# Performance work log

Measured on AMD Instinct MI355X. Metric: run time of the kernel, lower is better.

## Reference

```python
import jax, jax.numpy as jnp
import numpy as np

GROUPS = 1024
K_N = 32
FEAT_DIM = 64
EPS = 1e-05


def farthest_point_sample(xyz, npoint):
    # xyz: [B, N, 3] -> centroids [B, npoint] int32
    # Original torch code starts from a random point; we use index 0 for determinism.
    B, N, _ = xyz.shape

    def step(carry, _):
        distance, farthest = carry
        centroid = jnp.take_along_axis(xyz, farthest[:, None, None], axis=1)  # [B,1,3]
        dist = jnp.sum((xyz - centroid) ** 2, axis=-1)  # [B,N]
        distance = jnp.minimum(distance, dist)
        new_far = jnp.argmax(distance, axis=-1).astype(jnp.int32)
        return (distance, new_far), farthest

    init = (jnp.full((B, N), 1e10, dtype=xyz.dtype), jnp.zeros((B,), jnp.int32))
    _, cents = jax.lax.scan(step, init, None, length=npoint)
    return cents.T  # [B, npoint]


def index_points(points, idx):
    # points: [B, N, C]; idx: [B, ...] -> [B, ..., C]
    B = points.shape[0]
    bidx = jnp.arange(B).reshape((B,) + (1,) * (idx.ndim - 1))
    return points[bidx, idx]


def square_distance(src, dst):
    # src [B,S,C], dst [B,N,C] -> [B,S,N]
    d = -2.0 * jnp.einsum('bsc,bnc->bsn', src, dst)
    d = d + jnp.sum(src ** 2, -1)[:, :, None]
    d = d + jnp.sum(dst ** 2, -1)[:, None, :]
    return d


def setup_inputs() -> dict:
    key = jax.random.key(0)
    k1, k2 = jax.random.split(key)
    xyz = jax.random.normal(k1, (8, 3, 4096), dtype=jnp.float32)
    feats = jax.random.normal(k2, (8, FEAT_DIM, 4096), dtype=jnp.float32)
    affine_alpha_p = jnp.ones((1, 1, 1, FEAT_DIM), jnp.float32)
    affine_beta_p = jnp.zeros((1, 1, 1, FEAT_DIM), jnp.float32)
    return {"xyz": xyz, "feats": feats,
            "affine_alpha_p": affine_alpha_p, "affine_beta_p": affine_beta_p}


def reference(xyz, feats, affine_alpha_p, affine_beta_p):
    xyz = jnp.transpose(xyz, (0, 2, 1))      # [B,N,3]
    feats = jnp.transpose(feats, (0, 2, 1))  # [B,N,D]
    B, N, _ = xyz.shape
    S, k = GROUPS, K_N

    fps_idx = farthest_point_sample(xyz, S)          # [B,S]
    new_xyz = index_points(xyz, fps_idx)             # [B,S,3]
    new_feats = index_points(feats, fps_idx)         # [B,S,D]

    sqr = square_distance(new_xyz, xyz)              # [B,S,N]
    _, idx = jax.lax.top_k(-sqr, k)                  # smallest-k -> [B,S,k]
    grouped = index_points(feats, idx)               # [B,S,k,D]

    mean = new_feats[:, :, None, :]                  # [B,S,1,D]
    diff = grouped - mean
    # torch.std over flattened per-batch, unbiased (ddof=1)
    std = jnp.std(diff.reshape(B, -1), axis=-1, ddof=1)[:, None, None, None]
    grouped = diff / (std + EPS)
    grouped = affine_alpha_p * grouped + affine_beta_p

    point_feats = jnp.concatenate(
        [grouped, grouped - new_feats[:, :, None, :]], axis=-1)  # [B,S,k,2D]

    new_feats_out = jnp.transpose(new_feats, (0, 2, 1))          # [B,D,S]
    new_xyz_out = jnp.transpose(new_xyz, (0, 2, 1))              # [B,3,S]
    point_feats_out = jnp.transpose(point_feats, (0, 3, 1, 2))   # [B,2D,S,k]
    return (new_xyz_out, new_feats_out, point_feats_out)
```

## Files before the change

### kernel.cpp

```cpp
#include <hip/hip_runtime.h>

#define NPTS 4096
#define NSAMP 1024
#define KNN_K 32
#define FDIM 64
#define EPSF 1e-5f

#define DPP_MAX64(CTRL)                                                          \
  {                                                                              \
    unsigned _olo = (unsigned)__builtin_amdgcn_update_dpp(0, (int)klo, CTRL,     \
                                                          0xf, 0xf, true);       \
    unsigned _ohi = (unsigned)__builtin_amdgcn_update_dpp(0, (int)khi, CTRL,     \
                                                          0xf, 0xf, true);       \
    unsigned long long _ok = ((unsigned long long)_ohi << 32) | _olo;            \
    unsigned long long _ck = ((unsigned long long)khi << 32) | klo;              \
    if (_ok > _ck) { klo = _olo; khi = _ohi; }                                   \
  }

__global__ __launch_bounds__(256) void fps_kernel(const float* __restrict__ xyz,
                                                  int* __restrict__ fps_idx,
                                                  float* __restrict__ sqnorm) {
  __shared__ float4 pts[NPTS];
  __shared__ unsigned long long skeys[2][4];
  __shared__ int fpsb[NSAMP];
  const int b = blockIdx.x, t = threadIdx.x;
  const int lane = t & 63, w = t >> 6;
  const float* xb = xyz + (size_t)b * 3 * NPTS;
  float px[16], py[16], pz[16], dist[16];
  unsigned rik[16];
#pragma unroll
  for (int k = 0; k < 16; ++k) {
    int p = k * 256 + t;
    float x = xb[p], y = xb[NPTS + p], z = xb[2 * NPTS + p];
    float sq = __fadd_rn(__fadd_rn(__fmul_rn(x, x), __fmul_rn(y, y)),
                         __fmul_rn(z, z));
    px[k] = x; py[k] = y; pz[k] = z; dist[k] = 1e10f;
    rik[k] = 4095u - (unsigned)p;
    pts[p] = make_float4(x, y, z, sq);
    sqnorm[b * NPTS + p] = sq;
  }
  if (t == 0) fpsb[0] = 0;
  __syncthreads();
  float4 c = pts[0];
  for (int it = 1; it < NSAMP; ++it) {
#pragma unroll
    for (int k = 0; k < 16; ++k) {
      float dx = __fsub_rn(px[k], c.x);
      float dy = __fsub_rn(py[k], c.y);
      float dz = __fsub_rn(pz[k], c.z);
      float dd = __fadd_rn(__fadd_rn(__fmul_rn(dx, dx), __fmul_rn(dy, dy)),
                           __fmul_rn(dz, dz));
      dist[k] = fminf(dist[k], dd);
    }
    float m01 = fmaxf(dist[0], dist[1]),  m23 = fmaxf(dist[2], dist[3]);
    float m45 = fmaxf(dist[4], dist[5]),  m67 = fmaxf(dist[6], dist[7]);
    float m89 = fmaxf(dist[8], dist[9]),  mab = fmaxf(dist[10], dist[11]);
    float mcd = fmaxf(dist[12], dist[13]), mef = fmaxf(dist[14], dist[15]);
    float q0 = fmaxf(m01, m23), q1 = fmaxf(m45, m67);
    float q2 = fmaxf(m89, mab), q3 = fmaxf(mcd, mef);
    float mv = fmaxf(fmaxf(q0, q1), fmaxf(q2, q3));
    unsigned ri = rik[15];
#pragma unroll
    for (int k = 15; k >= 0; --k) ri = (dist[k] == mv) ? rik[k] : ri;
    unsigned bvb = __float_as_uint(mv);
    unsigned klo = (bvb << 12) | ri;
    unsigned khi = bvb >> 20;
    DPP_MAX64(0x111)
    DPP_MAX64(0x112)
    DPP_MAX64(0x114)
    DPP_MAX64(0x118)
    DPP_MAX64(0x142)
    DPP_MAX64(0x143)
    if (lane == 63) skeys[it & 1][w] = ((unsigned long long)khi << 32) | klo;
    __syncthreads();
    unsigned long long kk = skeys[it & 1][lane & 3];
    klo = (unsigned)kk;
    khi = (unsigned)(kk >> 32);
    DPP_MAX64(0x111)
    DPP_MAX64(0x112)
    unsigned flo = (unsigned)__builtin_amdgcn_readlane((int)klo, 3);
    int far = 4095 - (int)(flo & 0xfffu);
    if (t == 0) fpsb[it] = far;
    c = pts[far];
  }
  __syncthreads();
#pragma unroll
  for (int k = 0; k < 4; ++k)
    fps_idx[b * NSAMP + k * 256 + t] = fpsb[k * 256 + t];
}

__global__ __launch_bounds__(256) void gather_feats_kernel(const float* __restrict__ feats,
                                                           const int* __restrict__ fps,
                                                           float* __restrict__ out1,
                                                           float* __restrict__ nf) {
  int i = blockIdx.x * 256 + threadIdx.x;
  int s = i & 1023, c = (i >> 10) & 63, b = i >> 16;
  int p = fps[(b << 10) + s];
  float v = feats[((size_t)(b * 64 + c)) * NPTS + p];
  out1[(b * 64 + c) * 1024 + s] = v;
  nf[(((b << 10) + s) << 6) + c] = v;
}

__global__ __launch_bounds__(256) void gather_xyz_kernel(const float* __restrict__ xyz,
                                                         const float* __restrict__ sqnorm,
                                                         const int* __restrict__ fps,
                                                         float* __restrict__ out0,
                                                         float4* __restrict__ nx4) {
  int i = blockIdx.x * 256 + threadIdx.x;
  int b = i >> 10, s = i & 1023;
  int p = fps[i];
  const float* xb = xyz + (size_t)b * 3 * NPTS;
  float x = xb[p], y = xb[NPTS + p], z = xb[2 * NPTS + p];
  nx4[i] = make_float4(x, y, z, sqnorm[b * NPTS + p]);
  out0[(b * 3 + 0) * 1024 + s] = x;
  out0[(b * 3 + 1) * 1024 + s] = y;
  out0[(b * 3 + 2) * 1024 + s] = z;
}

__device__ __forceinline__ unsigned long long mk_key(float xn, float yn, float zn,
                                                     float sq, float cx, float cy,
                                                     float cz, float src2, int n) {
  float dot = __fmaf_rn(zn, cz, __fmaf_rn(yn, cy, __fmul_rn(xn, cx)));
  float d = __fadd_rn(__fadd_rn(__fmul_rn(-2.0f, dot), src2), sq);
  unsigned mb = __float_as_uint(d);
  mb = (mb & 0x80000000u) ? ~mb : (mb | 0x80000000u);
  return ((unsigned long long)mb << 32) | (unsigned)n;
}

__global__ __launch_bounds__(256, 2) void knn_kernel(const float* __restrict__ xyz,
                                                     const float* __restrict__ sqnorm,
                                                     const float4* __restrict__ nx4,
                                                     int* __restrict__ knn) {
  const int lane = threadIdx.x & 63;
  const int w = threadIdx.x >> 6;
  const int row = blockIdx.x * 4 + w;
  const int b = row >> 10;
  const float4 c4 = nx4[row];
  const float cx = c4.x, cy = c4.y, cz = c4.z, src2 = c4.w;
  const float4* x4 = (const float4*)(xyz + (size_t)b * 3 * NPTS);
  const float4* y4 = (const float4*)(xyz + (size_t)b * 3 * NPTS + NPTS);
  const float4* z4 = (const float4*)(xyz + (size_t)b * 3 * NPTS + 2 * NPTS);
  const float4* s4 = (const float4*)(sqnorm + (size_t)b * NPTS);
  unsigned long long key[64];
#pragma unroll
  for (int jj = 0; jj < 16; ++jj) {
    int vi = jj * 64 + lane;
    float4 xv = x4[vi], yv = y4[vi], zv = z4[vi], sv = s4[vi];
    int n0 = vi * 4;
    key[jj * 4 + 0] = mk_key(xv.x, yv.x, zv.x, sv.x, cx, cy, cz, src2, n0);
    key[jj * 4 + 1] = mk_key(xv.y, yv.y, zv.y, sv.y, cx, cy, cz, src2, n0 + 1);
    key[jj * 4 + 2] = mk_key(xv.z, yv.z, zv.z, sv.z, cx, cy, cz, src2, n0 + 2);
    key[jj * 4 + 3] = mk_key(xv.w, yv.w, zv.w, sv.w, cx, cy, cz, src2, n0 + 3);
  }
  unsigned long long last = 0ull;
  const int out_base = row * KNN_K;
#pragma unroll 1
  for (int r = 0; r < KNN_K; ++r) {
    unsigned long long cur = ~0ull;
#pragma unroll
    for (int j = 0; j < 64; ++j) {
      unsigned long long k = key[j];
      if (k > last && k < cur) cur = k;
    }
#pragma unroll
    for (int off = 32; off > 0; off >>= 1) {
      unsigned long long o = __shfl_xor(cur, off);
      cur = (o < cur) ? o : cur;
    }
    last = cur;
    if (lane == r) knn[out_base + r] = (int)(unsigned)(cur & 0xffffffffull);
  }
}

__global__ __launch_bounds__(256) void stats_kernel(const float* __restrict__ feats,
                                                    const float* __restrict__ nf,
                                                    const int* __restrict__ knn,
                                                    double* __restrict__ stats) {
  const int b = blockIdx.x >> 5;
  const int chunk = blockIdx.x & 31;
  const int base = chunk * 65536;
  double sm = 0.0, sq = 0.0;
  for (int i = 0; i < 256; ++i) {
    int e = base + i * 256 + threadIdx.x;
    int c = e >> 15;
    int sk = e & 32767;
    int s = sk >> 5, j = sk & 31;
    int p = knn[((((b << 10) + s)) << 5) + j];
    float f = feats[((size_t)(b * 64 + c)) * NPTS + p];
    float m = nf[(((b << 10) + s) << 6) + c];
    double d = (double)__fsub_rn(f, m);
    sm += d;
    sq += d * d;
  }
#pragma unroll
  for (int off = 32; off > 0; off >>= 1) {
    sm += __shfl_down(sm, off);
    sq += __shfl_down(sq, off);
  }
  __shared__ double red[8];
  int w = threadIdx.x >> 6;
  if ((threadIdx.x & 63) == 0) { red[w * 2] = sm; red[w * 2 + 1] = sq; }
  __syncthreads();
  if (threadIdx.x == 0) {
    atomicAdd(&stats[b * 2 + 0], red[0] + red[2] + red[4] + red[6]);
    atomicAdd(&stats[b * 2 + 1], red[1] + red[3] + red[5] + red[7]);
  }
}

__global__ __launch_bounds__(256) void out_kernel(const float* __restrict__ feats,
                                                  const float* __restrict__ nf,
                                                  const int* __restrict__ knn,
                                                  const double* __restrict__ stats,
                                                  const float* __restrict__ alpha,
                                                  const float* __restrict__ beta,
                                                  float* __restrict__ out2) {
  const int plane = blockIdx.x;
  const int b = plane >> 6, c = plane & 63;
  const int sk = blockIdx.y * 256 + threadIdx.x;
  const int s = sk >> 5, j = sk & 31;
  const double n = 2097152.0;
  double sm = stats[b * 2], sqs = stats[b * 2 + 1];
  double var = (sqs - sm * sm / n) / (n - 1.0);
  float stdf = (float)sqrt(var);
  float denom = stdf + EPSF;
  int p = knn[((((b << 10) + s)) << 5) + j];
  float f = feats[((size_t)(b * 64 + c)) * NPTS + p];
  float m = nf[(((b << 10) + s) << 6) + c];
  float diff = __fsub_rn(f, m);
  float g = alpha[c] * (diff / denom) + beta[c];
  size_t o1 = (((size_t)(b * 128 + c) << 10) + (size_t)s) * 32 + j;
  size_t o2 = (((size_t)(b * 128 + 64 + c) << 10) + (size_t)s) * 32 + j;
  out2[o1] = g;
  out2[o2] = g - m;
}

extern "C" void kernel_launch(void* const* d_in, const int* in_sizes, int n_in,
                              void* d_out, int out_size, void* d_ws, size_t ws_size,
                              hipStream_t stream) {
  (void)in_sizes; (void)n_in; (void)out_size; (void)ws_size;
  const float* xyz   = (const float*)d_in[0];
  const float* feats = (const float*)d_in[1];
  const float* alpha = (const float*)d_in[2];
  const float* beta  = (const float*)d_in[3];
  float* out  = (float*)d_out;
  float* out0 = out;
  float* out1 = out + 24576;
  float* out2 = out + 24576 + 524288;

  char* ws = (char*)d_ws;
  int*    fps   = (int*)ws;
  float*  sqn   = (float*)(ws + 32768);
  float4* nx4   = (float4*)(ws + 163840);
  float*  nf    = (float*)(ws + 294912);
  int*    knn   = (int*)(ws + 2392064);
  double* stats = (double*)(ws + 3440640);

  hipMemsetAsync(stats, 0, 128, stream);
  fps_kernel<<<8, 256, 0, stream>>>(xyz, fps, sqn);
  gather_feats_kernel<<<2048, 256, 0, stream>>>(feats, fps, out1, nf);
  gather_xyz_kernel<<<32, 256, 0, stream>>>(xyz, sqn, fps, out0, nx4);
  knn_kernel<<<2048, 256, 0, stream>>>(xyz, sqn, nx4, knn);
  stats_kernel<<<256, 256, 0, stream>>>(feats, nf, knn, stats);
  out_kernel<<<dim3(512, 128), 256, 0, stream>>>(feats, nf, knn, stats, alpha, beta, out2);
}
```

Measured before the change: 969.6 us.

## Pack two batches per FPS block and use float-max DPP with ballot argmax

The FPS kernel now runs two batches per 512-thread block (4 blocks instead of 8), and the per-wave argmax reduction is restructured. It first reduces only the float max across the wave with 32-bit DPP ops, then finds the index with a ballot over the 16 register slots. This replaces the 64-bit key DPP reduction and the per-lane index select. It cuts per-iteration ALU work in the serial FPS loop. Sharing one barrier across two batches may add sync coupling, and using fewer CUs gives no extra parallelism.

```diff
diff --git a/kernel.cpp b/kernel.cpp
--- a/kernel.cpp
+++ b/kernel.cpp
@@ -5,6 +5,13 @@
 #define KNN_K 32
 #define FDIM 64
 #define EPSF 1e-5f
+
+#define DPP_FMAX(CTRL)                                                           \
+  {                                                                              \
+    int _o = __builtin_amdgcn_update_dpp(0, __float_as_int(wv), CTRL, 0xf, 0xf,  \
+                                         true);                                  \
+    wv = fmaxf(wv, __int_as_float(_o));                                          \
+  }
 
 #define DPP_MAX64(CTRL)                                                          \
   {                                                                              \
@@ -17,31 +24,31 @@
     if (_ok > _ck) { klo = _olo; khi = _ohi; }                                   \
   }
 
-__global__ __launch_bounds__(256) void fps_kernel(const float* __restrict__ xyz,
+__global__ __launch_bounds__(512) void fps_kernel(const float* __restrict__ xyz,
                                                   int* __restrict__ fps_idx,
                                                   float* __restrict__ sqnorm) {
-  __shared__ float4 pts[NPTS];
-  __shared__ unsigned long long skeys[2][4];
-  __shared__ int fpsb[NSAMP];
-  const int b = blockIdx.x, t = threadIdx.x;
+  __shared__ float4 pts[2][NPTS];
+  __shared__ unsigned long long skeys[2][2][4];
+  __shared__ int fpsb[2][NSAMP];
+  const int t = threadIdx.x;
   const int lane = t & 63, w = t >> 6;
+  const int batch = w >> 2, wb = w & 3, lt = t & 255;
+  const int b = blockIdx.x * 2 + batch;
   const float* xb = xyz + (size_t)b * 3 * NPTS;
   float px[16], py[16], pz[16], dist[16];
-  unsigned rik[16];
 #pragma unroll
   for (int k = 0; k < 16; ++k) {
-    int p = k * 256 + t;
+    int p = k * 256 + lt;
     float x = xb[p], y = xb[NPTS + p], z = xb[2 * NPTS + p];
     float sq = __fadd_rn(__fadd_rn(__fmul_rn(x, x), __fmul_rn(y, y)),
                          __fmul_rn(z, z));
     px[k] = x; py[k] = y; pz[k] = z; dist[k] = 1e10f;
-    rik[k] = 4095u - (unsigned)p;
-    pts[p] = make_float4(x, y, z, sq);
+    pts[batch][p] = make_float4(x, y, z, sq);
     sqnorm[b * NPTS + p] = sq;
   }
-  if (t == 0) fpsb[0] = 0;
+  if (lt == 0) fpsb[batch][0] = 0;
   __syncthreads();
-  float4 c = pts[0];
+  float4 c = pts[batch][0];
   for (int it = 1; it < NSAMP; ++it) {
 #pragma unroll
     for (int k = 0; k < 16; ++k) {
@@ -58,35 +65,43 @@
     float mcd = fmaxf(dist[12], dist[13]), mef = fmaxf(dist[14], dist[15]);
     float q0 = fmaxf(m01, m23), q1 = fmaxf(m45, m67);
     float q2 = fmaxf(m89, mab), q3 = fmaxf(mcd, mef);
-    float mv = fmaxf(fmaxf(q0, q1), fmaxf(q2, q3));
-    unsigned ri = rik[15];
-#pragma unroll
-    for (int k = 15; k >= 0; --k) ri = (dist[k] == mv) ? rik[k] : ri;
-    unsigned bvb = __float_as_uint(mv);
-    unsigned klo = (bvb << 12) | ri;
-    unsigned khi = bvb >> 20;
-    DPP_MAX64(0x111)
-    DPP_MAX64(0x112)
-    DPP_MAX64(0x114)
-    DPP_MAX64(0x118)
-    DPP_MAX64(0x142)
-    DPP_MAX64(0x143)
-    if (lane == 63) skeys[it & 1][w] = ((unsigned long long)khi << 32) | klo;
+    float wv = fmaxf(fmaxf(q0, q1), fmaxf(q2, q3));
+    DPP_FMAX(0x111)
+    DPP_FMAX(0x112)
+    DPP_FMAX(0x114)
+    DPP_FMAX(0x118)
+    DPP_FMAX(0x142)
+    DPP_FMAX(0x143)
+    unsigned wvb = (unsigned)__builtin_amdgcn_readlane(__float_as_int(wv), 63);
+    float wvf = __uint_as_float(wvb);
+    int kk = 0, found = 0;
+    unsigned long long mm = 0ull;
+#pragma unroll
+    for (int k = 0; k < 16; ++k) {
+      unsigned long long m = __ballot(dist[k] == wvf);
+      if (!found && m != 0ull) { kk = k; mm = m; found = 1; }
+    }
+    int fl = __ffsll(mm) - 1;
+    int idx = kk * 256 + (wb << 6) + fl;
+    unsigned klo = (wvb << 12) | (4095u - (unsigned)idx);
+    unsigned khi = wvb >> 20;
+    if (lane == 0)
+      skeys[batch][it & 1][wb] = ((unsigned long long)khi << 32) | klo;
     __syncthreads();
-    unsigned long long kk = skeys[it & 1][lane & 3];
-    klo = (unsigned)kk;
-    khi = (unsigned)(kk >> 32);
+    unsigned long long kk2 = skeys[batch][it & 1][lane & 3];
+    klo = (unsigned)kk2;
+    khi = (unsigned)(kk2 >> 32);
     DPP_MAX64(0x111)
     DPP_MAX64(0x112)
     unsigned flo = (unsigned)__builtin_amdgcn_readlane((int)klo, 3);
     int far = 4095 - (int)(flo & 0xfffu);
-    if (t == 0) fpsb[it] = far;
-    c = pts[far];
+    if (lt == 0) fpsb[batch][it] = far;
+    c = pts[batch][far];
   }
   __syncthreads();
 #pragma unroll
   for (int k = 0; k < 4; ++k)
-    fps_idx[b * NSAMP + k * 256 + t] = fpsb[k * 256 + t];
+    fps_idx[b * NSAMP + k * 256 + lt] = fpsb[batch][k * 256 + lt];
 }
 
 __global__ __launch_bounds__(256) void gather_feats_kernel(const float* __restrict__ feats,
@@ -256,7 +271,7 @@
   double* stats = (double*)(ws + 3440640);
 
   hipMemsetAsync(stats, 0, 128, stream);
-  fps_kernel<<<8, 256, 0, stream>>>(xyz, fps, sqn);
+  fps_kernel<<<4, 512, 0, stream>>>(xyz, fps, sqn);
   gather_feats_kernel<<<2048, 256, 0, stream>>>(feats, fps, out1, nf);
   gather_xyz_kernel<<<32, 256, 0, stream>>>(xyz, sqn, fps, out0, nx4);
   knn_kernel<<<2048, 256, 0, stream>>>(xyz, sqn, nx4, knn);
```

Result: slower. 1.485 ms (+53.2%).
